# Kernel optimization log

Hardware: AMD Instinct MI355X
Metric: run time of the kernel (lower is better)

The kernel has to match this reference:

```python
import jax, jax.numpy as jnp
import numpy as np
from jax import lax

B, S, C = 128, 512, 16
V, CV = 50000, 100
E, CE = 100, 30
H = 128        # hidden per direction (hidden_dim=256 // 2)
T = 17         # tagset size
NF = 25        # filters per char-conv
LSTM_IN = E + 3 * NF  # 175


def setup_inputs() -> dict:
    key = jax.random.key(0)
    ks = jax.random.split(key, 25)
    sc = 0.1
    inp = {
        "x": jax.random.randint(ks[0], (B, S), 0, V),
        "char_x": jax.random.randint(ks[1], (B, S, C), 0, CV),
        "tags": jax.random.randint(ks[2], (B, S), 0, T),
        "mask": jnp.ones((B, S), dtype=bool),
        "word_emb": jax.random.normal(ks[3], (V, E), jnp.float32) * sc,
        "char_emb": jax.random.normal(ks[4], (CV, CE), jnp.float32) * sc,
        "conv2_W": jax.random.normal(ks[5], (NF, CE, 2), jnp.float32) * sc,
        "conv2_b": jnp.zeros((NF,), jnp.float32),
        "conv3_W": jax.random.normal(ks[6], (NF, CE, 3), jnp.float32) * sc,
        "conv3_b": jnp.zeros((NF,), jnp.float32),
        "conv4_W": jax.random.normal(ks[7], (NF, CE, 4), jnp.float32) * sc,
        "conv4_b": jnp.zeros((NF,), jnp.float32),
        "W_ih_f": jax.random.normal(ks[8], (4 * H, LSTM_IN), jnp.float32) * sc,
        "W_hh_f": jax.random.normal(ks[9], (4 * H, H), jnp.float32) * sc,
        "b_f": jnp.zeros((4 * H,), jnp.float32),
        "W_ih_b": jax.random.normal(ks[10], (4 * H, LSTM_IN), jnp.float32) * sc,
        "W_hh_b": jax.random.normal(ks[11], (4 * H, H), jnp.float32) * sc,
        "b_b": jnp.zeros((4 * H,), jnp.float32),
        "h2t_W": jax.random.normal(ks[12], (T, 2 * H), jnp.float32) * sc,
        "h2t_b": jnp.zeros((T,), jnp.float32),
        "crf_start": jax.random.normal(ks[13], (T,), jnp.float32) * sc,
        "crf_end": jax.random.normal(ks[14], (T,), jnp.float32) * sc,
        "crf_trans": jax.random.normal(ks[15], (T, T), jnp.float32) * sc,
    }
    return inp


def _char_conv(ce, W, b):
    # ce: [BS, CE, C], W: [O, I, K] -> [BS, O] after relu + max-over-time
    out = lax.conv_general_dilated(ce, W, (1,), 'VALID',
                                   dimension_numbers=('NCH', 'OIH', 'NCH'))
    out = jax.nn.relu(out + b[None, :, None])
    return jnp.max(out, axis=-1)


def _lstm_dir(xs, W_ih, W_hh, b, reverse):
    # xs: [B, S, D] -> hs [B, S, H]; PyTorch gate order i,f,g,o
    xs_t = jnp.swapaxes(xs, 0, 1)  # [S, B, D]
    if reverse:
        xs_t = xs_t[::-1]
    pre = jnp.einsum('sbd,gd->sbg', xs_t, W_ih) + b  # hoist input projection
    h0 = jnp.zeros((xs.shape[0], H), xs.dtype)

    def step(carry, p_t):
        h, c = carry
        g = p_t + h @ W_hh.T
        i = jax.nn.sigmoid(g[:, :H])
        f = jax.nn.sigmoid(g[:, H:2 * H])
        gg = jnp.tanh(g[:, 2 * H:3 * H])
        o = jax.nn.sigmoid(g[:, 3 * H:])
        c = f * c + i * gg
        h = o * jnp.tanh(c)
        return (h, c), h

    _, hs = lax.scan(step, (h0, h0), pre)
    if reverse:
        hs = hs[::-1]
    return jnp.swapaxes(hs, 0, 1)


def _crf_nll(emissions, tags, mask, start, end, trans):
    # emissions [B,S,T]; returns sum over batch of -log p(tags | emissions)
    maskf = mask.astype(emissions.dtype)
    # ---- numerator (gold score) ----
    em_sc = jnp.take_along_axis(emissions, tags[..., None], axis=2)[..., 0]  # [B,S]
    tr_sc = trans[tags[:, :-1], tags[:, 1:]]                                  # [B,S-1]
    last_idx = jnp.sum(mask, axis=1).astype(jnp.int32) - 1
    last_tag = tags[jnp.arange(tags.shape[0]), last_idx]
    score = (start[tags[:, 0]] + em_sc[:, 0]
             + jnp.sum(maskf[:, 1:] * (tr_sc + em_sc[:, 1:]), axis=1)
             + end[last_tag])
    # ---- partition via forward-algorithm scan ----
    em_t = jnp.swapaxes(emissions, 0, 1)  # [S,B,T]
    alpha0 = start[None, :] + em_t[0]     # [B,T]

    def step(alpha, inputs):
        e_t, m_t = inputs  # [B,T], [B]
        new = jax.nn.logsumexp(alpha[:, :, None] + trans[None] + e_t[:, None, :], axis=1)
        alpha = jnp.where(m_t[:, None], new, alpha)
        return alpha, None

    alpha, _ = lax.scan(step, alpha0, (em_t[1:], jnp.swapaxes(mask, 0, 1)[1:]))
    logZ = jax.nn.logsumexp(alpha + end[None, :], axis=1)
    return jnp.sum(logZ - score)


def reference(x, char_x, tags, mask, word_emb, char_emb,
              conv2_W, conv2_b, conv3_W, conv3_b, conv4_W, conv4_b,
              W_ih_f, W_hh_f, b_f, W_ih_b, W_hh_b, b_b,
              h2t_W, h2t_b, crf_start, crf_end, crf_trans):
    # word + char features
    we = word_emb[x]                                     # [B,S,E]
    ce = char_emb[char_x].reshape(B * S, C, CE)          # [BS,C,CE]
    ce = jnp.swapaxes(ce, 1, 2)                          # [BS,CE,C]
    cf = jnp.concatenate([_char_conv(ce, conv2_W, conv2_b),
                          _char_conv(ce, conv3_W, conv3_b),
                          _char_conv(ce, conv4_W, conv4_b)], axis=1)
    cf = cf.reshape(B, S, 3 * NF)
    feats = jnp.concatenate([we, cf], axis=2)            # [B,S,175]
    # BiLSTM
    h_fwd = _lstm_dir(feats, W_ih_f, W_hh_f, b_f, reverse=False)
    h_bwd = _lstm_dir(feats, W_ih_b, W_hh_b, b_b, reverse=True)
    h = jnp.concatenate([h_fwd, h_bwd], axis=2)          # [B,S,2H]
    emissions = jnp.einsum('bsh,th->bst', h, h2t_W) + h2t_b
    # CRF NLL (model returns -crf(...), torchcrf reduction='sum')
    return _crf_nll(emissions, tags, mask, crf_start, crf_end, crf_trans)
```

## Files before the change

### kernel.cpp

```cpp
#include <hip/hip_runtime.h>
#include <hip/hip_bf16.h>

#define B_ 128
#define S_ 512
#define C_ 16
#define E_ 100
#define CE_ 30
#define NF_ 25
#define H_ 128
#define T_ 17
#define LSTM_IN_ 175
#define KP_ 192
#define G4_ 512

typedef __hip_bfloat16 bf16;
typedef short bf16x8 __attribute__((ext_vector_type(8)));
typedef float f32x4 __attribute__((ext_vector_type(4)));

__device__ __forceinline__ float bf2f(unsigned short u){
  union { unsigned int i; float f; } v; v.i = ((unsigned int)u) << 16; return v.f;
}
__device__ __forceinline__ float sigm_f(float x){
  float e = __expf(-x);
  return __builtin_amdgcn_rcpf(1.0f + e);
}
__device__ __forceinline__ float tanh_f(float x){
  x = fminf(15.0f, fmaxf(-15.0f, x));
  float e = __expf(-2.0f*x);
  return (1.0f - e) * __builtin_amdgcn_rcpf(1.0f + e);
}
__device__ __forceinline__ short bf16bits(float f){
  bf16 b = __float2bfloat16(f);
  return *(short*)&b;
}

__global__ __launch_bounds__(256) void zero_pad_kernel(bf16* __restrict__ feats){
  int task = blockIdx.x*256 + threadIdx.x;
  int word = task / 17;
  int col = LSTM_IN_ + (task - word*17);
  feats[(size_t)word*KP_ + col] = __float2bfloat16(0.0f);
}

__global__ __launch_bounds__(256) void word_emb_kernel(const int* __restrict__ x,
    const float* __restrict__ wemb, bf16* __restrict__ feats){
  int word = blockIdx.x*2 + (threadIdx.x>>7);
  int e = threadIdx.x & 127;
  if (e < E_) feats[(size_t)word*KP_ + e] = __float2bfloat16(wemb[(size_t)x[word]*E_ + e]);
}

template<int KW>
__global__ __launch_bounds__(256) void char_conv_kernel(const int* __restrict__ char_x,
    const float* __restrict__ cemb, const float* __restrict__ W,
    const float* __restrict__ bias, bf16* __restrict__ feats, int out_off){
  int task = blockIdx.x*256 + threadIdx.x;
  int word = task / NF_;
  int fi = task - word*NF_;
  const int* cx = char_x + word*C_;
  float w[KW*CE_];
  #pragma unroll
  for (int i=0;i<KW*CE_;++i) w[i] = W[fi*CE_*KW + i];
  const int NP = C_ - KW + 1;
  float acc[C_ - KW + 1];
  #pragma unroll
  for (int p=0;p<NP;++p) acc[p] = 0.0f;
  #pragma unroll
  for (int c=0;c<C_;++c){
    int ci = cx[c];
    const float* ce = cemb + ci*CE_;
    #pragma unroll
    for (int e=0;e<CE_;++e){
      float v = ce[e];
      #pragma unroll
      for (int dx=0;dx<KW;++dx){
        int p = c - dx;
        if (p >= 0 && p < NP) acc[p] = fmaf(v, w[e*KW+dx], acc[p]);
      }
    }
  }
  float m = acc[0];
  #pragma unroll
  for (int p=1;p<NP;++p) m = fmaxf(m, acc[p]);
  feats[(size_t)word*KP_ + out_off + fi] = __float2bfloat16(fmaxf(0.0f, m + bias[fi]));
}

__global__ __launch_bounds__(192) void wpack_kernel(const float* __restrict__ Wf,
    const float* __restrict__ Wb, bf16* __restrict__ wpk){
  int g = blockIdx.x;
  int k = threadIdx.x;
  float v = 0.0f;
  if (k < LSTM_IN_) v = (g < 512) ? Wf[g*LSTM_IN_ + k] : Wb[(g-512)*LSTM_IN_ + k];
  wpk[(size_t)g*KP_ + k] = __float2bfloat16(v);
}

__global__ __launch_bounds__(256, 3) void pre_gemm_mfma(const bf16* __restrict__ feats,
    const bf16* __restrict__ wpk, const float* __restrict__ bf_,
    const float* __restrict__ bb_, bf16* __restrict__ pre){
  __shared__ __align__(16) short lds[16384];
  int br = blockIdx.x;
  int bc = blockIdx.y;
  int dir = bc >> 2;
  int g0 = (bc & 3) * 128;
  const float* bias = dir ? bb_ : bf_;
  int tid = threadIdx.x;
  int wave = tid >> 6, lane = tid & 63;
  int wr = wave >> 1, wc = wave & 1;
  int lrow = lane & 15, lkb = lane >> 4;
  const bf16* Arow = feats + (size_t)br*128*KP_;
  const bf16* Brow = wpk + (size_t)(dir*512 + g0)*KP_;

  auto stage = [&](int bufbase, int k0){
    int s0 = wave*2, s1 = s0 + 1;
    __builtin_amdgcn_global_load_lds(
        (const __attribute__((address_space(1))) void*)(Arow + (size_t)(s0*16 + lrow)*KP_ + k0 + lkb*8),
        (__attribute__((address_space(3))) void*)&lds[bufbase + s0*512], 16, 0, 0);
    __builtin_amdgcn_global_load_lds(
        (const __attribute__((address_space(1))) void*)(Arow + (size_t)(s1*16 + lrow)*KP_ + k0 + lkb*8),
        (__attribute__((address_space(3))) void*)&lds[bufbase + s1*512], 16, 0, 0);
    __builtin_amdgcn_global_load_lds(
        (const __attribute__((address_space(1))) void*)(Brow + (size_t)(s0*16 + lrow)*KP_ + k0 + lkb*8),
        (__attribute__((address_space(3))) void*)&lds[bufbase + 4096 + s0*512], 16, 0, 0);
    __builtin_amdgcn_global_load_lds(
        (const __attribute__((address_space(1))) void*)(Brow + (size_t)(s1*16 + lrow)*KP_ + k0 + lkb*8),
        (__attribute__((address_space(3))) void*)&lds[bufbase + 4096 + s1*512], 16, 0, 0);
  };

  f32x4 acc[4][4];
  #pragma unroll
  for (int i=0;i<4;++i)
    #pragma unroll
    for (int j=0;j<4;++j) acc[i][j] = (f32x4){0.f,0.f,0.f,0.f};

  stage(0, 0);
  __syncthreads();
  int cur = 0;
  for (int t = 0; t < 6; ++t){
    if (t < 5) stage((cur^1)*8192, (t+1)*32);
    const short* A  = &lds[cur*8192];
    const short* Bv = &lds[cur*8192 + 4096];
    bf16x8 af[4], bfr[4];
    #pragma unroll
    for (int i=0;i<4;++i) af[i]  = *(const bf16x8*)&A[(wr*4+i)*512 + lane*8];
    #pragma unroll
    for (int j=0;j<4;++j) bfr[j] = *(const bf16x8*)&Bv[(wc*4+j)*512 + lane*8];
    #pragma unroll
    for (int i=0;i<4;++i)
      #pragma unroll
      for (int j=0;j<4;++j)
        acc[i][j] = __builtin_amdgcn_mfma_f32_16x16x32_bf16(af[i], bfr[j], acc[i][j], 0, 0, 0);
    __syncthreads();
    cur ^= 1;
  }

  int col_l = lane & 15;
  int row_l = (lane >> 4) * 4;
  float bias_v[4];
  #pragma unroll
  for (int j=0;j<4;++j) bias_v[j] = bias[g0 + wc*64 + j*16 + col_l];
  #pragma unroll
  for (int i=0;i<4;++i){
    #pragma unroll
    for (int q=0;q<4;++q){
      int r = wr*64 + i*16 + row_l + q;
      #pragma unroll
      for (int j=0;j<4;++j){
        int cbyte = (wc*64 + j*16 + col_l) * 2;
        int addr = r*256 + (cbyte ^ ((r & 7) << 4));
        *(short*)((char*)lds + addr) = bf16bits(acc[i][j][q] + bias_v[j]);
      }
    }
  }
  __syncthreads();
  int r = tid >> 1, half = tid & 1;
  int word = br*128 + r;
  int bidx = word >> 9, sidx = word & 511;
  bf16* dst = pre + ((size_t)(dir*B_ + bidx)*S_ + sidx)*G4_ + g0 + half*64;
  #pragma unroll
  for (int k=0;k<8;++k){
    int boff = (half*128 + k*16) ^ ((r & 7) << 4);
    int4 v = *(const int4*)((const char*)lds + r*256 + boff);
    *(int4*)((char*)dst + k*16) = v;
  }
}

__global__ __launch_bounds__(512, 2) void lstm_kernel(const bf16* __restrict__ pre,
    const float* __restrict__ Whh_f, const float* __restrict__ Whh_b,
    bf16* __restrict__ hs){
  int blk = blockIdx.x;
  int dir = blk & 1;
  int b = blk >> 1;
  int g = threadIdx.x;
  const float* Whh = dir ? Whh_b : Whh_f;
  float w[128];
  {
    const float* Wrow = Whh + g*H_;
    #pragma unroll
    for (int k4=0;k4<32;++k4){
      float4 v = *(const float4*)&Wrow[k4*4];
      w[4*k4+0]=v.x; w[4*k4+1]=v.y; w[4*k4+2]=v.z; w[4*k4+3]=v.w;
    }
  }
  __shared__ __align__(16) float h_lds[H_];
  __shared__ float gates[G4_];
  if (g < H_) h_lds[g] = 0.0f;
  __syncthreads();
  const bf16* preB = pre + ((size_t)dir*B_ + b)*S_*G4_;
  bf16* hsB = hs + ((size_t)dir*B_ + b)*S_*H_;
  float c = 0.0f;
  int sect = g >> 7;
  float nxt = __bfloat162float(preB[(size_t)(dir ? (S_-1) : 0)*G4_ + g]);
  for (int s=0;s<S_;++s){
    int idx = dir ? (S_-1-s) : s;
    float pr = nxt;
    if (s+1 < S_){
      int idx1 = dir ? (S_-2-s) : (s+1);
      nxt = __bfloat162float(preB[(size_t)idx1*G4_ + g]);
    }
    float a0=0.f, a1=0.f, a2=0.f, a3=0.f;
    #pragma unroll
    for (int k4=0;k4<32;++k4){
      float4 h4 = *(const float4*)&h_lds[k4*4];
      a0 = fmaf(w[4*k4+0], h4.x, a0);
      a1 = fmaf(w[4*k4+1], h4.y, a1);
      a2 = fmaf(w[4*k4+2], h4.z, a2);
      a3 = fmaf(w[4*k4+3], h4.w, a3);
    }
    float acc = pr + ((a0+a1)+(a2+a3));
    float a = (sect == 2) ? tanh_f(acc) : sigm_f(acc);
    gates[g] = a;
    __syncthreads();
    if (g < H_){
      float iv = gates[g];
      float fv = gates[g+128];
      float gv = gates[g+256];
      float ov = gates[g+384];
      c = fmaf(fv, c, iv*gv);
      float hn = ov * tanh_f(c);
      h_lds[g] = hn;
      hsB[(size_t)idx*H_ + g] = __float2bfloat16(hn);
    }
    __syncthreads();
  }
}

__global__ __launch_bounds__(256) void emis_kernel(const bf16* __restrict__ hs,
    const float* __restrict__ W, const float* __restrict__ bias, float* __restrict__ em){
  int task = blockIdx.x*256 + threadIdx.x;
  int word = task / T_;
  int t = task - word*T_;
  const ushort4* hf = (const ushort4*)(hs + (size_t)word*H_);
  const ushort4* hb = (const ushort4*)(hs + (size_t)(B_*S_ + word)*H_);
  const float* w0 = W + t*2*H_;
  float acc = bias[t];
  #pragma unroll
  for (int j4=0;j4<32;++j4){
    ushort4 u = hf[j4];
    float4 w4 = *(const float4*)&w0[j4*4];
    acc = fmaf(bf2f(u.x),w4.x,acc); acc = fmaf(bf2f(u.y),w4.y,acc);
    acc = fmaf(bf2f(u.z),w4.z,acc); acc = fmaf(bf2f(u.w),w4.w,acc);
  }
  #pragma unroll
  for (int j4=0;j4<32;++j4){
    ushort4 u = hb[j4];
    float4 w4 = *(const float4*)&w0[H_ + j4*4];
    acc = fmaf(bf2f(u.x),w4.x,acc); acc = fmaf(bf2f(u.y),w4.y,acc);
    acc = fmaf(bf2f(u.z),w4.z,acc); acc = fmaf(bf2f(u.w),w4.w,acc);
  }
  em[(size_t)word*T_ + t] = acc;
}

__global__ __launch_bounds__(256) void score_kernel(const int* __restrict__ tags,
    const float* __restrict__ em, const float* __restrict__ start,
    const float* __restrict__ end_, const float* __restrict__ trans,
    float* __restrict__ score){
  int b = blockIdx.x;
  int tid = threadIdx.x;
  const int* tg = tags + b*S_;
  const float* eb = em + (size_t)b*S_*T_;
  float s = 0.0f;
  for (int t = tid; t < S_; t += 256){
    int cur = tg[t];
    s += eb[(size_t)t*T_ + cur];
    if (t > 0) s += trans[tg[t-1]*T_ + cur];
  }
  if (tid == 0) s += start[tg[0]] + end_[tg[S_-1]];
  __shared__ float red[256];
  red[tid] = s; __syncthreads();
  for (int off=128; off; off>>=1){
    if (tid < off) red[tid] += red[tid+off];
    __syncthreads();
  }
  if (tid == 0) score[b] = red[0];
}

__global__ __launch_bounds__(64) void crf_alpha_kernel(const float* __restrict__ em,
    const float* __restrict__ start, const float* __restrict__ end_,
    const float* __restrict__ trans, float* __restrict__ logZ){
  int b = blockIdx.x;
  int j = threadIdx.x;
  __shared__ float al[T_];
  const float* eb = em + (size_t)b*S_*T_;
  float tcol[T_];
  if (j < T_){
    #pragma unroll
    for (int i=0;i<T_;++i) tcol[i] = trans[i*T_ + j];
    al[j] = start[j] + eb[j];
  }
  __syncthreads();
  float e_cur = (j < T_) ? eb[T_ + j] : 0.0f;
  for (int s=1;s<S_;++s){
    float e_nxt = (j < T_ && s+1 < S_) ? eb[(size_t)(s+1)*T_ + j] : 0.0f;
    float nv = 0.0f;
    if (j < T_){
      float av[T_];
      float m = -1e30f;
      #pragma unroll
      for (int i=0;i<T_;++i){ av[i] = al[i] + tcol[i]; m = fmaxf(m, av[i]); }
      float sum = 0.0f;
      #pragma unroll
      for (int i=0;i<T_;++i) sum += __expf(av[i]-m);
      nv = m + __logf(sum) + e_cur;
    }
    __syncthreads();
    if (j < T_) al[j] = nv;
    __syncthreads();
    e_cur = e_nxt;
  }
  if (j == 0){
    float m = -1e30f;
    float v[T_];
    #pragma unroll
    for (int i=0;i<T_;++i){ v[i] = al[i] + end_[i]; m = fmaxf(m, v[i]); }
    float sum = 0.0f;
    #pragma unroll
    for (int i=0;i<T_;++i) sum += __expf(v[i]-m);
    logZ[b] = m + __logf(sum);
  }
}

__global__ __launch_bounds__(128) void final_kernel(const float* __restrict__ logZ,
    const float* __restrict__ score, float* __restrict__ out){
  int tid = threadIdx.x;
  float v = logZ[tid] - score[tid];
  __shared__ float red[128];
  red[tid] = v; __syncthreads();
  for (int off=64; off; off>>=1){
    if (tid < off) red[tid] += red[tid+off];
    __syncthreads();
  }
  if (tid == 0) out[0] = red[0];
}

extern "C" void kernel_launch(void* const* d_in, const int* in_sizes, int n_in,
                              void* d_out, int out_size, void* d_ws, size_t ws_size,
                              hipStream_t stream) {
  const int*   x       = (const int*)  d_in[0];
  const int*   char_x  = (const int*)  d_in[1];
  const int*   tags    = (const int*)  d_in[2];
  const float* wemb    = (const float*)d_in[4];
  const float* cemb    = (const float*)d_in[5];
  const float* c2W     = (const float*)d_in[6];
  const float* c2b     = (const float*)d_in[7];
  const float* c3W     = (const float*)d_in[8];
  const float* c3b     = (const float*)d_in[9];
  const float* c4W     = (const float*)d_in[10];
  const float* c4b     = (const float*)d_in[11];
  const float* Wih_f   = (const float*)d_in[12];
  const float* Whh_f   = (const float*)d_in[13];
  const float* b_f     = (const float*)d_in[14];
  const float* Wih_b   = (const float*)d_in[15];
  const float* Whh_b   = (const float*)d_in[16];
  const float* b_b     = (const float*)d_in[17];
  const float* h2tW    = (const float*)d_in[18];
  const float* h2tb    = (const float*)d_in[19];
  const float* crf_s   = (const float*)d_in[20];
  const float* crf_e   = (const float*)d_in[21];
  const float* crf_t   = (const float*)d_in[22];
  float* out = (float*)d_out;

  const size_t NEEDED = 167773184ULL;
  if (ws_size < NEEDED) return;
  char* wsb = (char*)d_ws;
  bf16*  pre   = (bf16*)(wsb);
  bf16*  feats = (bf16*)(wsb + 134217728);
  bf16*  wpk   = (bf16*)(wsb + 159383552);
  bf16*  hs    = (bf16*)(wsb + 134217728);
  float* em    = (float*)(wsb);
  float* score = (float*)(wsb + 167772160);
  float* logZ  = (float*)(wsb + 167772672);

  zero_pad_kernel<<<4352, 256, 0, stream>>>(feats);
  word_emb_kernel<<<32768, 256, 0, stream>>>(x, wemb, feats);
  char_conv_kernel<2><<<6400, 256, 0, stream>>>(char_x, cemb, c2W, c2b, feats, E_);
  char_conv_kernel<3><<<6400, 256, 0, stream>>>(char_x, cemb, c3W, c3b, feats, E_ + NF_);
  char_conv_kernel<4><<<6400, 256, 0, stream>>>(char_x, cemb, c4W, c4b, feats, E_ + 2*NF_);
  wpack_kernel<<<1024, 192, 0, stream>>>(Wih_f, Wih_b, wpk);
  pre_gemm_mfma<<<dim3(512, 8), 256, 0, stream>>>(feats, wpk, b_f, b_b, pre);
  lstm_kernel<<<256, 512, 0, stream>>>(pre, Whh_f, Whh_b, hs);
  emis_kernel<<<4352, 256, 0, stream>>>(hs, h2tW, h2tb, em);
  score_kernel<<<128, 256, 0, stream>>>(tags, em, crf_s, crf_e, crf_t, score);
  crf_alpha_kernel<<<128, 64, 0, stream>>>(em, crf_s, crf_e, crf_t, logZ);
  final_kernel<<<1, 128, 0, stream>>>(logZ, score, out);
}
```

Baseline: 1.580 ms.

## Batch LSTM recurrence over 16 sequences per block using bf16 MFMA

The recurrent step now has one block handle 16 batch rows, so 16 blocks replace 256. Each block computes h·W_hhᵀ with bf16 MFMA instructions, keeping W_hh fragments in registers and h in swizzled LDS. Gate preactivations are prefetched two steps ahead. The change removes the per-thread scalar FMA dot products and the per-step gate exchange through LDS, but occupies only 16 of the GPU's CUs and lowers the recurrent weights and hidden state to bf16, which may cost accuracy.

Result: slower. 1.675 ms (+6.0%).

```diff
diff --git a/kernel.cpp b/kernel.cpp
--- a/kernel.cpp
+++ b/kernel.cpp
@@ -90,6 +90,15 @@
   float v = 0.0f;
   if (k < LSTM_IN_) v = (g < 512) ? Wf[g*LSTM_IN_ + k] : Wb[(g-512)*LSTM_IN_ + k];
   wpk[(size_t)g*KP_ + k] = __float2bfloat16(v);
+}
+
+__global__ __launch_bounds__(256) void whh_pack_kernel(const float* __restrict__ Wf,
+    const float* __restrict__ Wb, bf16* __restrict__ wpk2){
+  int idx = blockIdx.x*256 + threadIdx.x;
+  int dir = idx >> 16;
+  int rem = idx & 65535;
+  const float* W = dir ? Wb : Wf;
+  wpk2[idx] = __float2bfloat16(W[rem]);
 }
 
 __global__ __launch_bounds__(256, 3) void pre_gemm_mfma(const bf16* __restrict__ feats,
@@ -182,63 +191,94 @@
   }
 }
 
-__global__ __launch_bounds__(512, 2) void lstm_kernel(const bf16* __restrict__ pre,
-    const float* __restrict__ Whh_f, const float* __restrict__ Whh_b,
+__global__ __launch_bounds__(512, 2) void lstm_mfma_kernel(
+    const bf16* __restrict__ pre, const bf16* __restrict__ wpk2,
     bf16* __restrict__ hs){
   int blk = blockIdx.x;
   int dir = blk & 1;
-  int b = blk >> 1;
-  int g = threadIdx.x;
-  const float* Whh = dir ? Whh_b : Whh_f;
-  float w[128];
+  int bg  = blk >> 1;
+  int tid = threadIdx.x;
+  int w = tid >> 6, l = tid & 63;
+  int lm = l & 15, lk = l >> 4;
+  int gcol = 16*w + lm;
+
+  bf16x8 Bf[4][4];
   {
-    const float* Wrow = Whh + g*H_;
-    #pragma unroll
-    for (int k4=0;k4<32;++k4){
-      float4 v = *(const float4*)&Wrow[k4*4];
-      w[4*k4+0]=v.x; w[4*k4+1]=v.y; w[4*k4+2]=v.z; w[4*k4+3]=v.w;
-    }
-  }
-  __shared__ __align__(16) float h_lds[H_];
-  __shared__ float gates[G4_];
-  if (g < H_) h_lds[g] = 0.0f;
+    const bf16* Wd = wpk2 + (size_t)dir*512*128;
+    #pragma unroll
+    for (int ct=0; ct<4; ++ct)
+      #pragma unroll
+      for (int kk=0; kk<4; ++kk)
+        Bf[ct][kk] = *(const bf16x8*)(Wd + (ct*128 + gcol)*128 + 32*kk + lk*8);
+  }
+
+  __shared__ __align__(16) short h_sh[2048];
+  for (int i = tid; i < 1024; i += 512) ((int*)h_sh)[i] = 0;
+
+  float c[4] = {0.f, 0.f, 0.f, 0.f};
+  const bf16* preB = pre + (size_t)(dir*B_ + bg*16) * (S_*G4_);
+  bf16* hsB = hs + (size_t)(dir*B_ + bg*16) * (S_*H_);
+
+  unsigned short pfA[16], pfB[16];
+  auto LOADPF = [&](unsigned short (&pf)[16], int idx){
+    #pragma unroll
+    for (int q=0;q<4;++q){
+      #pragma unroll
+      for (int ct=0;ct<4;++ct)
+        pf[q*4+ct] = *(const unsigned short*)(preB
+            + ((size_t)((lk*4+q)*S_ + idx))*G4_ + ct*128 + gcol);
+    }
+  };
+
+  auto STEP = [&](unsigned short (&pfuse)[16], int s){
+    int idx = dir ? (S_-1-s) : s;
+    f32x4 a0, a1, a2, a3;
+    #pragma unroll
+    for (int q=0;q<4;++q){
+      a0[q] = bf2f(pfuse[q*4+0]);
+      a1[q] = bf2f(pfuse[q*4+1]);
+      a2[q] = bf2f(pfuse[q*4+2]);
+      a3[q] = bf2f(pfuse[q*4+3]);
+    }
+    int sp = (s+2 < S_) ? s+2 : s;
+    int idxp = dir ? (S_-1-sp) : sp;
+    LOADPF(pfuse, idxp);
+    #pragma unroll
+    for (int kk=0;kk<4;++kk){
+      int sc = ((4*kk + lk) ^ lm) & 15;
+      bf16x8 af = *(const bf16x8*)((const char*)h_sh + lm*256 + sc*16);
+      a0 = __builtin_amdgcn_mfma_f32_16x16x32_bf16(af, Bf[0][kk], a0, 0, 0, 0);
+      a1 = __builtin_amdgcn_mfma_f32_16x16x32_bf16(af, Bf[1][kk], a1, 0, 0, 0);
+      a2 = __builtin_amdgcn_mfma_f32_16x16x32_bf16(af, Bf[2][kk], a2, 0, 0, 0);
+      a3 = __builtin_amdgcn_mfma_f32_16x16x32_bf16(af, Bf[3][kk], a3, 0, 0, 0);
+    }
+    float hv[4];
+    #pragma unroll
+    for (int q=0;q<4;++q){
+      float iv = sigm_f(a0[q]);
+      float fv = sigm_f(a1[q]);
+      float gv = tanh_f(a2[q]);
+      float ov = sigm_f(a3[q]);
+      c[q] = fmaf(fv, c[q], iv*gv);
+      hv[q] = ov * tanh_f(c[q]);
+    }
+    __syncthreads();
+    #pragma unroll
+    for (int q=0;q<4;++q){
+      int b = lk*4 + q;
+      int scw = ((gcol >> 3) ^ b) & 15;
+      *(short*)((char*)h_sh + b*256 + scw*16 + (gcol & 7)*2) = bf16bits(hv[q]);
+      hsB[((size_t)b*S_ + idx)*H_ + gcol] = __float2bfloat16(hv[q]);
+    }
+    __syncthreads();
+  };
+
   __syncthreads();
-  const bf16* preB = pre + ((size_t)dir*B_ + b)*S_*G4_;
-  bf16* hsB = hs + ((size_t)dir*B_ + b)*S_*H_;
-  float c = 0.0f;
-  int sect = g >> 7;
-  float nxt = __bfloat162float(preB[(size_t)(dir ? (S_-1) : 0)*G4_ + g]);
-  for (int s=0;s<S_;++s){
-    int idx = dir ? (S_-1-s) : s;
-    float pr = nxt;
-    if (s+1 < S_){
-      int idx1 = dir ? (S_-2-s) : (s+1);
-      nxt = __bfloat162float(preB[(size_t)idx1*G4_ + g]);
-    }
-    float a0=0.f, a1=0.f, a2=0.f, a3=0.f;
-    #pragma unroll
-    for (int k4=0;k4<32;++k4){
-      float4 h4 = *(const float4*)&h_lds[k4*4];
-      a0 = fmaf(w[4*k4+0], h4.x, a0);
-      a1 = fmaf(w[4*k4+1], h4.y, a1);
-      a2 = fmaf(w[4*k4+2], h4.z, a2);
-      a3 = fmaf(w[4*k4+3], h4.w, a3);
-    }
-    float acc = pr + ((a0+a1)+(a2+a3));
-    float a = (sect == 2) ? tanh_f(acc) : sigm_f(acc);
-    gates[g] = a;
-    __syncthreads();
-    if (g < H_){
-      float iv = gates[g];
-      float fv = gates[g+128];
-      float gv = gates[g+256];
-      float ov = gates[g+384];
-      c = fmaf(fv, c, iv*gv);
-      float hn = ov * tanh_f(c);
-      h_lds[g] = hn;
-      hsB[(size_t)idx*H_ + g] = __float2bfloat16(hn);
-    }
-    __syncthreads();
+  LOADPF(pfA, dir ? (S_-1) : 0);
+  LOADPF(pfB, dir ? (S_-2) : 1);
+  for (int s = 0; s < S_; s += 2){
+    STEP(pfA, s);
+    STEP(pfB, s+1);
   }
 }
 
@@ -377,7 +417,7 @@
   const float* crf_t   = (const float*)d_in[22];
   float* out = (float*)d_out;
 
-  const size_t NEEDED = 167773184ULL;
+  const size_t NEEDED = 168035328ULL;
   if (ws_size < NEEDED) return;
   char* wsb = (char*)d_ws;
   bf16*  pre   = (bf16*)(wsb);
@@ -387,6 +427,7 @@
   float* em    = (float*)(wsb);
   float* score = (float*)(wsb + 167772160);
   float* logZ  = (float*)(wsb + 167772672);
+  bf16*  wpk2  = (bf16*)(wsb + 167773184);
 
   zero_pad_kernel<<<4352, 256, 0, stream>>>(feats);
   word_emb_kernel<<<32768, 256, 0, stream>>>(x, wemb, feats);
@@ -394,8 +435,9 @@
   char_conv_kernel<3><<<6400, 256, 0, stream>>>(char_x, cemb, c3W, c3b, feats, E_ + NF_);
   char_conv_kernel<4><<<6400, 256, 0, stream>>>(char_x, cemb, c4W, c4b, feats, E_ + 2*NF_);
   wpack_kernel<<<1024, 192, 0, stream>>>(Wih_f, Wih_b, wpk);
+  whh_pack_kernel<<<512, 256, 0, stream>>>(Whh_f, Whh_b, wpk2);
   pre_gemm_mfma<<<dim3(512, 8), 256, 0, stream>>>(feats, wpk, b_f, b_b, pre);
-  lstm_kernel<<<256, 512, 0, stream>>>(pre, Whh_f, Whh_b, hs);
+  lstm_mfma_kernel<<<16, 512, 0, stream>>>(pre, wpk2, hs);
   emis_kernel<<<4352, 256, 0, stream>>>(hs, h2tW, h2tb, em);
   score_kernel<<<128, 256, 0, stream>>>(tags, em, crf_s, crf_e, crf_t, score);
   crf_alpha_kernel<<<128, 64, 0, stream>>>(em, crf_s, crf_e, crf_t, logZ);
```
